# Kernel tuning notes

Measured on AMD Instinct MI355X. Metric: run time of the kernel, lower is better.

Reference implementation:

```python
import jax, jax.numpy as jnp
import numpy as np

DIM = 1024
NUM_HEADS = 16
HEAD_DIM = DIM // NUM_HEADS
WINDOW = 128
EPS = 1e-5


def setup_inputs() -> dict:
    key = jax.random.key(0)
    ks = jax.random.split(key, 8)
    B, S, D = 1, 2048, DIM
    x = jax.random.normal(ks[0], (B, S, D), dtype=jnp.float32)
    # xavier-uniform-ish scale for linear weights (torch layout: [out, in])
    def xavier(k, out_f, in_f):
        lim = np.sqrt(6.0 / (in_f + out_f)).astype(np.float32)
        return jax.random.uniform(k, (out_f, in_f), jnp.float32, -lim, lim)
    qkv_w = xavier(ks[1], 3 * D, D)
    out_w = xavier(ks[2], D, D)
    ln_g = jnp.ones((D,), jnp.float32)
    ln_b = jnp.zeros((D,), jnp.float32)
    w1 = xavier(ks[3], 4 * D, D)
    b1 = jnp.zeros((4 * D,), jnp.float32)
    w2 = xavier(ks[4], D, 4 * D)
    b2 = jnp.zeros((D,), jnp.float32)
    return {"x": x, "qkv_w": qkv_w, "out_w": out_w, "ln_g": ln_g,
            "ln_b": ln_b, "w1": w1, "b1": b1, "w2": w2, "b2": b2}


def reference(x, qkv_w, out_w, ln_g, ln_b, w1, b1, w2, b2):
    B, S, D = x.shape
    H, hd = NUM_HEADS, HEAD_DIM
    residual = x
    # LayerNorm (pre-norm)
    mu = jnp.mean(x, axis=-1, keepdims=True)
    var = jnp.var(x, axis=-1, keepdims=True)
    xn = (x - mu) * jax.lax.rsqrt(var + EPS) * ln_g + ln_b
    # QKV projection (torch Linear: y = x @ W^T)
    qkv = xn @ qkv_w.T                              # [B,S,3D]
    qkv = qkv.reshape(B, S, 3, H, hd).transpose(2, 0, 3, 1, 4)  # [3,B,H,S,hd]
    q, k, v = qkv[0], qkv[1], qkv[2]
    # Local-window boolean mask: |i - j| <= window_size // 2
    w = WINDOW // 2
    i = jnp.arange(S)[:, None]
    j = jnp.arange(S)[None, :]
    local_mask = jnp.abs(i - j) <= w                # [S,S]
    # SDPA with boolean mask
    scale = 1.0 / np.sqrt(hd).astype(np.float32)
    scores = jnp.einsum('bhqd,bhkd->bhqk', q, k) * scale
    scores = jnp.where(local_mask, scores, -jnp.inf)
    attn = jax.nn.softmax(scores, axis=-1)
    attn_out = jnp.einsum('bhqk,bhkd->bhqd', attn, v)
    attn_out = attn_out.transpose(0, 2, 1, 3).reshape(B, S, D)
    attn_out = attn_out @ out_w.T
    out = residual + attn_out
    # FFN (no second norm in this module), exact GELU
    h = jax.nn.gelu(out @ w1.T + b1, approximate=False)
    ffn_out = h @ w2.T + b2
    return out + ffn_out
```

## Files before the change

kernel.cpp:

```cpp
#include <hip/hip_runtime.h>
#include <math.h>

typedef unsigned short u16;
typedef __attribute__((ext_vector_type(8))) short short8;
typedef __attribute__((ext_vector_type(4))) float f32x4;
typedef __attribute__((ext_vector_type(4))) int i32x4;
typedef __attribute__((ext_vector_type(4))) u16 u16x4;

__device__ inline u16 f2bf(float f){
  union { float f; unsigned int u; } x; x.f = f;
  unsigned int r = x.u + 0x7fffu + ((x.u >> 16) & 1u);
  return (u16)(r >> 16);
}

__global__ __launch_bounds__(256) void prep_kernel(
    const float* __restrict__ x, const float* __restrict__ g, const float* __restrict__ b,
    u16* __restrict__ xn,
    const float* __restrict__ qkv_w, u16* __restrict__ qkvw_b,
    const float* __restrict__ out_w, u16* __restrict__ outw_b,
    const float* __restrict__ w1,    u16* __restrict__ w1_b,
    const float* __restrict__ w2,    u16* __restrict__ w2_b)
{
  const int tid = threadIdx.x;
  int bid = blockIdx.x;
  if (bid < 2048){
    const int row = bid;
    float4 v = *(const float4*)(x + (size_t)row*1024 + tid*4);
    float s  = v.x + v.y + v.z + v.w;
    float ss = v.x*v.x + v.y*v.y + v.z*v.z + v.w*v.w;
    #pragma unroll
    for (int off = 32; off; off >>= 1){
      s  += __shfl_xor(s,  off, 64);
      ss += __shfl_xor(ss, off, 64);
    }
    __shared__ float red[8];
    const int wid = tid >> 6;
    if ((tid & 63) == 0){ red[wid] = s; red[4+wid] = ss; }
    __syncthreads();
    float S  = red[0]+red[1]+red[2]+red[3];
    float SS = red[4]+red[5]+red[6]+red[7];
    float mu  = S * (1.0f/1024.0f);
    float var = SS * (1.0f/1024.0f) - mu*mu;
    float rs  = rsqrtf(var + 1e-5f);
    float4 gv = *(const float4*)(g + tid*4);
    float4 bv = *(const float4*)(b + tid*4);
    u16x4 pk;
    pk.x = f2bf((v.x-mu)*rs*gv.x + bv.x);
    pk.y = f2bf((v.y-mu)*rs*gv.y + bv.y);
    pk.z = f2bf((v.z-mu)*rs*gv.z + bv.z);
    pk.w = f2bf((v.w-mu)*rs*gv.w + bv.w);
    *(u16x4*)(xn + (size_t)row*1024 + tid*4) = pk;
    return;
  }
  bid -= 2048;
  const float* src; u16* dst;
  if (bid < 3072){ src = qkv_w; dst = qkvw_b; }
  else if (bid < 3072+1024){ src = out_w; dst = outw_b; bid -= 3072; }
  else if (bid < 3072+1024+4096){ src = w1; dst = w1_b; bid -= 3072+1024; }
  else { src = w2; dst = w2_b; bid -= 3072+1024+4096; }
  const size_t i = ((size_t)bid*256 + tid) * 4;
  float4 v = *(const float4*)(src + i);
  u16x4 pk;
  pk.x = f2bf(v.x); pk.y = f2bf(v.y); pk.z = f2bf(v.z); pk.w = f2bf(v.w);
  *(u16x4*)(dst + i) = pk;
}

template<int EPI, int BN>
__global__ __launch_bounds__(256) void gemm_lds(
    const u16* __restrict__ A, const u16* __restrict__ B,
    float* __restrict__ outF, u16* __restrict__ outB,
    const float* __restrict__ bias, const float* __restrict__ resid,
    int M, int N, int K, int nbx, int nwg, int Kc)
{
  constexpr int NR = BN / 32;
  __shared__ u16 As[2][128*64];
  __shared__ u16 Bs[2][BN*64];
  const int tid = threadIdx.x;
  const int l   = tid & 63;
  const int w   = tid >> 6;
  const int wr  = w >> 1, wc = w & 1;
  const int orig = blockIdx.x;
  const int wgid = (orig & 7) * (nwg >> 3) + (orig >> 3);
  const int bcol = wgid % nbx, brow = wgid / nbx;
  const int kz = blockIdx.y;
  const int l15 = l & 15, l4 = l >> 4;

  const u16* Ab = A + (size_t)brow*128*K + (size_t)kz*Kc;
  const u16* Bb = B + (size_t)bcol*BN*K  + (size_t)kz*Kc;

  f32x4 acc[4][NR];
  #pragma unroll
  for (int i = 0; i < 4; ++i)
    #pragma unroll
    for (int j = 0; j < NR; ++j)
      acc[i][j] = (f32x4){0.f, 0.f, 0.f, 0.f};

  const int rsub = l >> 3;
  const int csrc = ((l & 7) ^ rsub) * 8;
  const int swz  = (l15 & 7) * 8;
  const int nkt = Kc >> 6;

  auto stage = [&](int kt, int buf){
    const u16* Ag = Ab + kt*64 + csrc;
    const u16* Bg = Bb + kt*64 + csrc;
    #pragma unroll
    for (int i = 0; i < 4; ++i){
      const int ca = w*4 + i;
      __builtin_amdgcn_global_load_lds(
        (const __attribute__((address_space(1))) void*)(Ag + (size_t)(ca*8 + rsub)*K),
        (__attribute__((address_space(3))) void*)(&As[buf][ca*512]), 16, 0, 0);
    }
    #pragma unroll
    for (int i = 0; i < NR; ++i){
      const int cb = w*NR + i;
      __builtin_amdgcn_global_load_lds(
        (const __attribute__((address_space(1))) void*)(Bg + (size_t)(cb*8 + rsub)*K),
        (__attribute__((address_space(3))) void*)(&Bs[buf][cb*512]), 16, 0, 0);
    }
  };

  stage(0, 0);
  __syncthreads();
  for (int kt = 0; kt < nkt; ++kt){
    const int cur = kt & 1;
    if (kt + 1 < nkt) stage(kt + 1, cur ^ 1);
    #pragma unroll
    for (int ks = 0; ks < 2; ++ks){
      const int kop = (ks*32 + l4*8) ^ swz;
      short8 af[4], bfr[NR];
      #pragma unroll
      for (int i = 0; i < 4; ++i)  af[i]  = *(const short8*)&As[cur][(wr*64 + i*16 + l15)*64 + kop];
      #pragma unroll
      for (int j = 0; j < NR; ++j) bfr[j] = *(const short8*)&Bs[cur][(wc*(BN/2) + j*16 + l15)*64 + kop];
      #pragma unroll
      for (int i = 0; i < 4; ++i)
        #pragma unroll
        for (int j = 0; j < NR; ++j)
          acc[i][j] = __builtin_amdgcn_mfma_f32_16x16x32_bf16(af[i], bfr[j], acc[i][j], 0, 0, 0);
    }
    __syncthreads();
  }

  #pragma unroll
  for (int i = 0; i < 4; ++i){
    #pragma unroll
    for (int j = 0; j < NR; ++j){
      #pragma unroll
      for (int r = 0; r < 4; ++r){
        int row = brow*128 + wr*64 + i*16 + l4*4 + r;
        int col = bcol*BN + wc*(BN/2) + j*16 + l15;
        float v = acc[i][j][r];
        size_t o = (size_t)row * N + col;
        if constexpr (EPI == 0){
          outB[o] = f2bf(v);
        } else if constexpr (EPI == 1){
          v += resid[o];
          outF[o] = v;
          outB[o] = f2bf(v);
        } else if constexpr (EPI == 2){
          v += bias[col];
          v = 0.5f * v * (1.0f + erff(v * 0.70710678118654752f));
          outB[o] = f2bf(v);
        } else {
          outF[(size_t)kz * M * N + o] = v;
        }
      }
    }
  }
}

__global__ __launch_bounds__(256) void reduce_ffn2(const float* __restrict__ p,
                                                   const float* __restrict__ bias,
                                                   const float* __restrict__ resid,
                                                   float* __restrict__ out){
  const size_t s = (size_t)2048*1024;
  const size_t i = ((size_t)blockIdx.x * 256 + threadIdx.x) * 4;
  float4 a0 = *(const float4*)(p + i);
  float4 a1 = *(const float4*)(p + s + i);
  float4 a2 = *(const float4*)(p + 2*s + i);
  float4 a3 = *(const float4*)(p + 3*s + i);
  float4 r  = *(const float4*)(resid + i);
  float4 bb = *(const float4*)(bias + (i & 1023));
  float4 o;
  o.x = a0.x + a1.x + a2.x + a3.x + r.x + bb.x;
  o.y = a0.y + a1.y + a2.y + a3.y + r.y + bb.y;
  o.z = a0.z + a1.z + a2.z + a3.z + r.z + bb.z;
  o.w = a0.w + a1.w + a2.w + a3.w + r.w + bb.w;
  *(float4*)(out + i) = o;
}

__global__ __launch_bounds__(256) void attn_kernel(const u16* __restrict__ qkv, u16* __restrict__ attn_out){
  constexpr int S = 2048, D3 = 3072;
  const int qt = blockIdx.x, h = blockIdx.y;
  const int q0 = qt * 64;
  const int tid = threadIdx.x;
  const int l = tid & 63, w = tid >> 6;
  const int l15 = l & 15, l4 = l >> 4;

  __shared__ u16 smem[31232];
  u16 (*Qs)[72]  = (u16(*)[72]) (smem);
  u16 (*Ks)[72]  = (u16(*)[72]) (smem + 4608);
  u16 (*Ps)[200] = (u16(*)[200])(smem + 4608);
  u16 (*Vt)[200] = (u16(*)[200])(smem + 18432);

  #pragma unroll
  for (int i = 0; i < 2; ++i){
    int cid = tid + 256*i; int r = cid >> 3, c = cid & 7;
    *(i32x4*)&Qs[r][c*8] = *(const i32x4*)(qkv + (size_t)(q0 + r)*D3 + h*64 + c*8);
  }
  #pragma unroll
  for (int i = 0; i < 6; ++i){
    int cid = tid + 256*i; int r = cid >> 3, c = cid & 7;
    int kj = q0 - 64 + r;
    i32x4 kv = {0,0,0,0}, vv = {0,0,0,0};
    if (kj >= 0 && kj < S){
      kv = *(const i32x4*)(qkv + (size_t)kj*D3 + 1024 + h*64 + c*8);
      vv = *(const i32x4*)(qkv + (size_t)kj*D3 + 2048 + h*64 + c*8);
    }
    *(i32x4*)&Ks[r][c*8] = kv;
    union { i32x4 v; u16 u[8]; } uu; uu.v = vv;
    #pragma unroll
    for (int j = 0; j < 8; ++j) Vt[c*8 + j][r] = uu.u[j];
  }
  __syncthreads();

  f32x4 sc[12];
  #pragma unroll
  for (int cf = 0; cf < 12; ++cf) sc[cf] = (f32x4){0.f,0.f,0.f,0.f};
  const int ko = l4 * 8;
  short8 a0 = *(const short8*)&Qs[16*w + l15][ko];
  short8 a1 = *(const short8*)&Qs[16*w + l15][32 + ko];
  #pragma unroll
  for (int cf = 0; cf < 12; ++cf){
    short8 b0 = *(const short8*)&Ks[cf*16 + l15][ko];
    short8 b1 = *(const short8*)&Ks[cf*16 + l15][32 + ko];
    sc[cf] = __builtin_amdgcn_mfma_f32_16x16x32_bf16(a0, b0, sc[cf], 0, 0, 0);
    sc[cf] = __builtin_amdgcn_mfma_f32_16x16x32_bf16(a1, b1, sc[cf], 0, 0, 0);
  }
  __syncthreads();

  const float scale = 0.125f;
  #pragma unroll
  for (int r = 0; r < 4; ++r){
    const int qrl = 16*w + l4*4 + r;
    float mx = -1e30f;
    #pragma unroll
    for (int cf = 0; cf < 12; ++cf){
      int j  = cf*16 + l15;
      int kj = q0 - 64 + j;
      bool ok = (j >= qrl) && (j <= qrl + 128) && (kj >= 0) && (kj < S);
      float sv = ok ? sc[cf][r]*scale : -1e30f;
      sc[cf][r] = sv;
      mx = fmaxf(mx, sv);
    }
    #pragma unroll
    for (int off = 1; off < 16; off <<= 1) mx = fmaxf(mx, __shfl_xor(mx, off, 64));
    float sm = 0.f;
    #pragma unroll
    for (int cf = 0; cf < 12; ++cf){
      float pv = __expf(sc[cf][r] - mx);
      sc[cf][r] = pv;
      sm += pv;
    }
    #pragma unroll
    for (int off = 1; off < 16; off <<= 1) sm += __shfl_xor(sm, off, 64);
    float inv = 1.0f / sm;
    #pragma unroll
    for (int cf = 0; cf < 12; ++cf) Ps[qrl][cf*16 + l15] = f2bf(sc[cf][r] * inv);
  }
  __syncthreads();

  f32x4 o[4];
  #pragma unroll
  for (int df = 0; df < 4; ++df) o[df] = (f32x4){0.f,0.f,0.f,0.f};
  #pragma unroll
  for (int kk = 0; kk < 6; ++kk){
    short8 a = *(const short8*)&Ps[16*w + l15][kk*32 + ko];
    #pragma unroll
    for (int df = 0; df < 4; ++df){
      short8 b = *(const short8*)&Vt[df*16 + l15][kk*32 + ko];
      o[df] = __builtin_amdgcn_mfma_f32_16x16x32_bf16(a, b, o[df], 0, 0, 0);
    }
  }
  #pragma unroll
  for (int df = 0; df < 4; ++df){
    #pragma unroll
    for (int r = 0; r < 4; ++r){
      attn_out[(size_t)(q0 + 16*w + l4*4 + r)*1024 + h*64 + df*16 + l15] = f2bf(o[df][r]);
    }
  }
}

extern "C" void kernel_launch(void* const* d_in, const int* in_sizes, int n_in,
                              void* d_out, int out_size, void* d_ws, size_t ws_size,
                              hipStream_t stream)
{
  const float* x     = (const float*)d_in[0];
  const float* qkv_w = (const float*)d_in[1];
  const float* out_w = (const float*)d_in[2];
  const float* ln_g  = (const float*)d_in[3];
  const float* ln_b  = (const float*)d_in[4];
  const float* w1    = (const float*)d_in[5];
  const float* b1    = (const float*)d_in[6];
  const float* w2    = (const float*)d_in[7];
  const float* b2    = (const float*)d_in[8];
  float* out_final = (float*)d_out;

  char* p = (char*)d_ws;
  u16* xn_b   = (u16*)p; p += (size_t)2048*1024*2;
  u16* qkv_b  = (u16*)p; p += (size_t)2048*3072*2;
  u16* attn_b = (u16*)p; p += (size_t)2048*1024*2;
  u16* out_b  = (u16*)p; p += (size_t)2048*1024*2;
  u16* qkvw_b = (u16*)p; p += (size_t)3072*1024*2;
  u16* outw_b = (u16*)p; p += (size_t)1024*1024*2;
  u16* w1_b   = (u16*)p; p += (size_t)4096*1024*2;
  u16* w2_b   = (u16*)p; p += (size_t)1024*4096*2;
  float* out_f= (float*)p; p += (size_t)2048*1024*4;
  u16* h_b    = (u16*)p; p += (size_t)2048*4096*2;

  float* partials = (float*)xn_b;

  prep_kernel<<<14336, 256, 0, stream>>>(x, ln_g, ln_b, xn_b,
                                         qkv_w, qkvw_b, out_w, outw_b,
                                         w1, w1_b, w2, w2_b);
  gemm_lds<0,64><<<dim3(768), 256, 0, stream>>>(xn_b, qkvw_b, nullptr, qkv_b, nullptr, nullptr,
                                                2048, 3072, 1024, 48, 768, 1024);
  attn_kernel<<<dim3(32,16), 256, 0, stream>>>(qkv_b, attn_b);
  gemm_lds<1,64><<<dim3(256), 256, 0, stream>>>(attn_b, outw_b, out_f, out_b, nullptr, x,
                                                2048, 1024, 1024, 16, 256, 1024);
  gemm_lds<2,128><<<dim3(512), 256, 0, stream>>>(out_b, w1_b, nullptr, h_b, b1, nullptr,
                                                 2048, 4096, 1024, 32, 512, 1024);
  gemm_lds<4,128><<<dim3(128, 4), 256, 0, stream>>>(h_b, w2_b, partials, nullptr, nullptr, nullptr,
                                                    2048, 1024, 4096, 8, 128, 1024);
  reduce_ffn2<<<2048, 256, 0, stream>>>(partials, b2, out_f, out_final);
}
```

Baseline: 129.0 us.

## Use tanh GELU, bf16 residual, async swizzled K loads in attention

Replaces exact erf GELU in the FFN1 epilogue with a tanh-approximation built on exp. Drops the fp32 copy of the attention residual and feeds the bf16 copy into the final reduce, cutting epilogue writes and reduce reads. K tiles in attention now load via global_load_lds with an XOR swizzle, and shared memory is shrunk. Both the bf16 residual and the approximate GELU lower precision relative to the exact reference. The async K load also drops the bounds check for the first and last query tiles, so rows outside the sequence are read.

```diff
diff --git a/kernel.cpp b/kernel.cpp
--- a/kernel.cpp
+++ b/kernel.cpp
@@ -7,10 +7,22 @@
 typedef __attribute__((ext_vector_type(4))) int i32x4;
 typedef __attribute__((ext_vector_type(4))) u16 u16x4;
 
+#define AS1 __attribute__((address_space(1)))
+#define AS3 __attribute__((address_space(3)))
+
 __device__ inline u16 f2bf(float f){
   union { float f; unsigned int u; } x; x.f = f;
   unsigned int r = x.u + 0x7fffu + ((x.u >> 16) & 1u);
   return (u16)(r >> 16);
+}
+__device__ inline float bf2f(u16 u){
+  union { unsigned int u; float f; } x; x.u = ((unsigned int)u) << 16;
+  return x.f;
+}
+__device__ inline float gelu_fast(float v){
+  float y = 0.7978845608f * (v + 0.044715f * v * v * v);
+  float e = __expf(2.0f * y);
+  return v - v / (e + 1.0f);
 }
 
 __global__ __launch_bounds__(256) void prep_kernel(
@@ -107,15 +119,15 @@
     for (int i = 0; i < 4; ++i){
       const int ca = w*4 + i;
       __builtin_amdgcn_global_load_lds(
-        (const __attribute__((address_space(1))) void*)(Ag + (size_t)(ca*8 + rsub)*K),
-        (__attribute__((address_space(3))) void*)(&As[buf][ca*512]), 16, 0, 0);
+        (const AS1 void*)(Ag + (size_t)(ca*8 + rsub)*K),
+        (AS3 void*)(&As[buf][ca*512]), 16, 0, 0);
     }
     #pragma unroll
     for (int i = 0; i < NR; ++i){
       const int cb = w*NR + i;
       __builtin_amdgcn_global_load_lds(
-        (const __attribute__((address_space(1))) void*)(Bg + (size_t)(cb*8 + rsub)*K),
-        (__attribute__((address_space(3))) void*)(&Bs[buf][cb*512]), 16, 0, 0);
+        (const AS1 void*)(Bg + (size_t)(cb*8 + rsub)*K),
+        (AS3 void*)(&Bs[buf][cb*512]), 16, 0, 0);
     }
   };
 
@@ -155,12 +167,10 @@
           outB[o] = f2bf(v);
         } else if constexpr (EPI == 1){
           v += resid[o];
-          outF[o] = v;
           outB[o] = f2bf(v);
         } else if constexpr (EPI == 2){
           v += bias[col];
-          v = 0.5f * v * (1.0f + erff(v * 0.70710678118654752f));
-          outB[o] = f2bf(v);
+          outB[o] = f2bf(gelu_fast(v));
         } else {
           outF[(size_t)kz * M * N + o] = v;
         }
@@ -171,7 +181,7 @@
 
 __global__ __launch_bounds__(256) void reduce_ffn2(const float* __restrict__ p,
                                                    const float* __restrict__ bias,
-                                                   const float* __restrict__ resid,
+                                                   const u16* __restrict__ resid_b,
                                                    float* __restrict__ out){
   const size_t s = (size_t)2048*1024;
   const size_t i = ((size_t)blockIdx.x * 256 + threadIdx.x) * 4;
@@ -179,13 +189,13 @@
   float4 a1 = *(const float4*)(p + s + i);
   float4 a2 = *(const float4*)(p + 2*s + i);
   float4 a3 = *(const float4*)(p + 3*s + i);
-  float4 r  = *(const float4*)(resid + i);
+  u16x4 rb  = *(const u16x4*)(resid_b + i);
   float4 bb = *(const float4*)(bias + (i & 1023));
   float4 o;
-  o.x = a0.x + a1.x + a2.x + a3.x + r.x + bb.x;
-  o.y = a0.y + a1.y + a2.y + a3.y + r.y + bb.y;
-  o.z = a0.z + a1.z + a2.z + a3.z + r.z + bb.z;
-  o.w = a0.w + a1.w + a2.w + a3.w + r.w + bb.w;
+  o.x = a0.x + a1.x + a2.x + a3.x + bf2f(rb.x) + bb.x;
+  o.y = a0.y + a1.y + a2.y + a3.y + bf2f(rb.y) + bb.y;
+  o.z = a0.z + a1.z + a2.z + a3.z + bf2f(rb.z) + bb.z;
+  o.w = a0.w + a1.w + a2.w + a3.w + bf2f(rb.w) + bb.w;
   *(float4*)(out + i) = o;
 }
 
@@ -197,27 +207,36 @@
   const int l = tid & 63, w = tid >> 6;
   const int l15 = l & 15, l4 = l >> 4;
 
-  __shared__ u16 smem[31232];
+  __shared__ u16 smem[29696];
   u16 (*Qs)[72]  = (u16(*)[72]) (smem);
-  u16 (*Ks)[72]  = (u16(*)[72]) (smem + 4608);
-  u16 (*Ps)[200] = (u16(*)[200])(smem + 4608);
-  u16 (*Vt)[200] = (u16(*)[200])(smem + 18432);
+  u16 *Ks        = smem + 4608;
+  u16 (*Ps)[200] = (u16(*)[200])(smem);
+  u16 (*Vt)[200] = (u16(*)[200])(smem + 16896);
 
   #pragma unroll
   for (int i = 0; i < 2; ++i){
     int cid = tid + 256*i; int r = cid >> 3, c = cid & 7;
     *(i32x4*)&Qs[r][c*8] = *(const i32x4*)(qkv + (size_t)(q0 + r)*D3 + h*64 + c*8);
   }
+  {
+    const int rsubK = l >> 3;
+    const int csrcK = ((l & 7) ^ rsubK) * 8;
+    #pragma unroll
+    for (int i = 0; i < 6; ++i){
+      const int ca = w*6 + i;
+      const long kj = (long)(q0 - 64 + ca*8 + rsubK);
+      __builtin_amdgcn_global_load_lds(
+        (const AS1 void*)(qkv + kj*D3 + 1024 + h*64 + csrcK),
+        (AS3 void*)(Ks + ca*512), 16, 0, 0);
+    }
+  }
   #pragma unroll
   for (int i = 0; i < 6; ++i){
     int cid = tid + 256*i; int r = cid >> 3, c = cid & 7;
     int kj = q0 - 64 + r;
-    i32x4 kv = {0,0,0,0}, vv = {0,0,0,0};
-    if (kj >= 0 && kj < S){
-      kv = *(const i32x4*)(qkv + (size_t)kj*D3 + 1024 + h*64 + c*8);
+    i32x4 vv = {0,0,0,0};
+    if (kj >= 0 && kj < S)
       vv = *(const i32x4*)(qkv + (size_t)kj*D3 + 2048 + h*64 + c*8);
-    }
-    *(i32x4*)&Ks[r][c*8] = kv;
     union { i32x4 v; u16 u[8]; } uu; uu.v = vv;
     #pragma unroll
     for (int j = 0; j < 8; ++j) Vt[c*8 + j][r] = uu.u[j];
@@ -228,12 +247,13 @@
   #pragma unroll
   for (int cf = 0; cf < 12; ++cf) sc[cf] = (f32x4){0.f,0.f,0.f,0.f};
   const int ko = l4 * 8;
+  const int swzK = (l15 & 7) * 8;
   short8 a0 = *(const short8*)&Qs[16*w + l15][ko];
   short8 a1 = *(const short8*)&Qs[16*w + l15][32 + ko];
   #pragma unroll
   for (int cf = 0; cf < 12; ++cf){
-    short8 b0 = *(const short8*)&Ks[cf*16 + l15][ko];
-    short8 b1 = *(const short8*)&Ks[cf*16 + l15][32 + ko];
+    short8 b0 = *(const short8*)&Ks[(cf*16 + l15)*64 + (ko ^ swzK)];
+    short8 b1 = *(const short8*)&Ks[(cf*16 + l15)*64 + ((32 + ko) ^ swzK)];
     sc[cf] = __builtin_amdgcn_mfma_f32_16x16x32_bf16(a0, b0, sc[cf], 0, 0, 0);
     sc[cf] = __builtin_amdgcn_mfma_f32_16x16x32_bf16(a1, b1, sc[cf], 0, 0, 0);
   }
@@ -315,10 +335,9 @@
   u16* outw_b = (u16*)p; p += (size_t)1024*1024*2;
   u16* w1_b   = (u16*)p; p += (size_t)4096*1024*2;
   u16* w2_b   = (u16*)p; p += (size_t)1024*4096*2;
-  float* out_f= (float*)p; p += (size_t)2048*1024*4;
   u16* h_b    = (u16*)p; p += (size_t)2048*4096*2;
 
-  float* partials = (float*)xn_b;
+  float* partials = (float*)p;
 
   prep_kernel<<<14336, 256, 0, stream>>>(x, ln_g, ln_b, xn_b,
                                          qkv_w, qkvw_b, out_w, outw_b,
@@ -326,11 +345,11 @@
   gemm_lds<0,64><<<dim3(768), 256, 0, stream>>>(xn_b, qkvw_b, nullptr, qkv_b, nullptr, nullptr,
                                                 2048, 3072, 1024, 48, 768, 1024);
   attn_kernel<<<dim3(32,16), 256, 0, stream>>>(qkv_b, attn_b);
-  gemm_lds<1,64><<<dim3(256), 256, 0, stream>>>(attn_b, outw_b, out_f, out_b, nullptr, x,
+  gemm_lds<1,64><<<dim3(256), 256, 0, stream>>>(attn_b, outw_b, nullptr, out_b, nullptr, x,
                                                 2048, 1024, 1024, 16, 256, 1024);
   gemm_lds<2,128><<<dim3(512), 256, 0, stream>>>(out_b, w1_b, nullptr, h_b, b1, nullptr,
                                                  2048, 4096, 1024, 32, 512, 1024);
   gemm_lds<4,128><<<dim3(128, 4), 256, 0, stream>>>(h_b, w2_b, partials, nullptr, nullptr, nullptr,
                                                     2048, 1024, 4096, 8, 128, 1024);
-  reduce_ffn2<<<2048, 256, 0, stream>>>(partials, b2, out_f, out_final);
-}
+  reduce_ffn2<<<2048, 256, 0, stream>>>(partials, b2, out_b, out_final);
+}
```

Result: faster. 124.1 us (-3.8%).
